# Kernel optimization log

Measured on AMD Instinct MI355X. Metric: run time of the kernel, lower is better.

## Reference

```python
import jax, jax.numpy as jnp
import numpy as np

S, DIM, H = 2048, 1024, 16
D = DIM // H  # head_dim = 64


def rope_rotate_half(x):
    x1, x2 = jnp.split(x, 2, axis=-1)
    return jnp.concatenate([-x2, x1], axis=-1)


def setup_inputs() -> dict:
    key = jax.random.key(0)
    ks = jax.random.split(key, 8)
    x = jax.random.normal(ks[0], (S, DIM), dtype=jnp.float32)
    # RoPE tables for full sequence (HW == S, prefix == 0)
    pos = jnp.arange(S, dtype=jnp.float32)[:, None]
    inv_freq = 1.0 / (10000.0 ** (jnp.arange(0, D, 2, dtype=jnp.float32) / D))
    ang = pos * inv_freq[None, :]                      # [S, D/2]
    ang = jnp.concatenate([ang, ang], axis=-1)         # [S, D]
    sin, cos = jnp.sin(ang), jnp.cos(ang)
    # equinox Linear: weight [out, in], y = W @ x + b
    W_qkv = jax.random.normal(ks[1], (3 * DIM, DIM), dtype=jnp.float32) * (DIM ** -0.5)
    b_qkv = jnp.zeros((3 * DIM,), dtype=jnp.float32)
    W_proj = jax.random.normal(ks[2], (DIM, DIM), dtype=jnp.float32) * (DIM ** -0.5)
    b_proj = jnp.zeros((DIM,), dtype=jnp.float32)
    return {"x": x, "sin": sin, "cos": cos, "W_qkv": W_qkv, "b_qkv": b_qkv,
            "W_proj": W_proj, "b_proj": b_proj}


def reference(x, sin, cos, W_qkv, b_qkv, W_proj, b_proj):
    # fused QKV projection: [S, 3*DIM]
    qkv = x @ W_qkv.T + b_qkv
    # 's (n h d) -> n h s d'
    qkv = qkv.reshape(S, 3, H, D).transpose(1, 2, 0, 3)
    q, k, v = qkv[0], qkv[1], qkv[2]                   # each [H, S, D]
    # qk_norm = False -> Identity. RoPE over all S tokens (prefix = 0).
    sin_b, cos_b = sin[None, :, :], cos[None, :, :]    # [1, S, D]
    q = q * cos_b + rope_rotate_half(q) * sin_b
    k = k * cos_b + rope_rotate_half(k) * sin_b
    attn = jnp.einsum('hqd,hkd->hqk', q, k) / jnp.sqrt(jnp.float32(D))
    attn = jax.nn.softmax(attn, axis=-1)               # [H, S, S]
    out = jnp.einsum('hqk,hkd->hqd', attn, v)          # [H, S, D]
    out = out.transpose(1, 0, 2).reshape(S, DIM)       # 'h s d -> s (h d)'
    return out @ W_proj.T + b_proj
```

## Files before the change

kernel.cpp:

```cpp
#include <hip/hip_runtime.h>

#define S_LEN 2048
#define DIM 1024
#define NH 16
#define HD 64
#define KSPLIT 4

typedef __attribute__((ext_vector_type(8))) __bf16 bf16x8;
typedef __attribute__((ext_vector_type(4))) _Float16 f16x4;
typedef __attribute__((ext_vector_type(4))) float f32x4;
typedef __attribute__((ext_vector_type(8))) unsigned short us8;
typedef __attribute__((ext_vector_type(4))) unsigned short us4;

__device__ __forceinline__ unsigned short f2bf(float f) {
    union { float f; unsigned u; } v; v.f = f;
    unsigned r = v.u + 0x7FFFu + ((v.u >> 16) & 1u);
    return (unsigned short)(r >> 16);
}
__device__ __forceinline__ float bf2f(unsigned short h) {
    union { unsigned u; float f; } v; v.u = ((unsigned)h) << 16;
    return v.f;
}
__device__ __forceinline__ f32x4 mfma16(bf16x8 a, bf16x8 b, f32x4 c) {
    return __builtin_amdgcn_mfma_f32_16x16x32_bf16(a, b, c, 0, 0, 0);
}
__device__ __forceinline__ f32x4 mfma16h(f16x4 a, f16x4 b, f32x4 c) {
    return __builtin_amdgcn_mfma_f32_16x16x16f16(a, b, c, 0, 0, 0);
}
__device__ __forceinline__ void gload_lds16(void* lds, const void* g) {
    __builtin_amdgcn_global_load_lds(
        (__attribute__((address_space(1))) void*)const_cast<void*>(g),
        (__attribute__((address_space(3))) void*)lds, 16, 0, 0);
}

__global__ __launch_bounds__(256) void convert2_kernel(
    const float* __restrict__ a, unsigned short* __restrict__ oa,
    const float* __restrict__ b, unsigned short* __restrict__ ob)
{
    const int bid = blockIdx.x;
    const float* in;
    unsigned short* out;
    int i;
    if (bid < 1024) { in = a; out = oa; i = (bid * 256 + threadIdx.x) * 8; }
    else            { in = b; out = ob; i = ((bid - 1024) * 256 + threadIdx.x) * 8; }
    const float4 p = *(const float4*)(in + i);
    const float4 q = *(const float4*)(in + i + 4);
    us8 o;
    o[0] = f2bf(p.x); o[1] = f2bf(p.y); o[2] = f2bf(p.z); o[3] = f2bf(p.w);
    o[4] = f2bf(q.x); o[5] = f2bf(q.y); o[6] = f2bf(q.z); o[7] = f2bf(q.w);
    *(us8*)(out + i) = o;
}

__global__ __launch_bounds__(256) void gemm_qkv_kernel(
    const unsigned short* __restrict__ A, const unsigned short* __restrict__ B,
    const float* __restrict__ bias, unsigned short* __restrict__ C,
    int M, int N, int K)
{
    __shared__ __align__(16) unsigned short As[128 * 32];
    __shared__ __align__(16) unsigned short Bs[64 * 32];

    const int tid  = threadIdx.x;
    const int w    = tid >> 6;
    const int lane = tid & 63;
    const int quad = lane >> 4;
    const int l15  = lane & 15;
    const int bm = blockIdx.y * 128, bn = blockIdx.x * 64;
    const int wm = w * 32;
    const int srow = lane >> 2;
    const int skc  = (lane & 3) * 8;

    f32x4 acc[2][4];
    const f32x4 zero4 = {0.f, 0.f, 0.f, 0.f};
    #pragma unroll
    for (int i = 0; i < 2; ++i)
        #pragma unroll
        for (int j = 0; j < 4; ++j) acc[i][j] = zero4;

    for (int k0 = 0; k0 < K; k0 += 32) {
        __syncthreads();
        #pragma unroll
        for (int t = 0; t < 2; ++t) {
            const int row = w * 32 + t * 16 + srow;
            gload_lds16(&As[(w * 32 + t * 16) * 32],
                        A + (size_t)(bm + row) * K + k0 + skc);
        }
        gload_lds16(&Bs[(w * 16) * 32],
                    B + (size_t)(bn + w * 16 + srow) * K + k0 + skc);
        __syncthreads();

        bf16x8 a[2], b[4];
        #pragma unroll
        for (int i = 0; i < 2; ++i)
            a[i] = *(const bf16x8*)&As[(wm + 16 * i + l15) * 32 + quad * 8];
        #pragma unroll
        for (int j = 0; j < 4; ++j)
            b[j] = *(const bf16x8*)&Bs[(16 * j + l15) * 32 + quad * 8];
        #pragma unroll
        for (int i = 0; i < 2; ++i)
            #pragma unroll
            for (int j = 0; j < 4; ++j)
                acc[i][j] = mfma16(a[i], b[j], acc[i][j]);
    }

    #pragma unroll
    for (int j = 0; j < 4; ++j) {
        const int col = bn + 16 * j + l15;
        const float bv = bias[col];
        #pragma unroll
        for (int i = 0; i < 2; ++i)
            #pragma unroll
            for (int r = 0; r < 4; ++r) {
                const int row = bm + wm + 16 * i + quad * 4 + r;
                C[(size_t)row * N + col] = f2bf(acc[i][j][r] + bv);
            }
    }
}

__global__ __launch_bounds__(256) void rope_vtrans_kernel(
    unsigned short* __restrict__ qkv, const float* __restrict__ sin_t,
    const float* __restrict__ cos_t, _Float16* __restrict__ Vt)
{
    const int bid = blockIdx.x;
    if (bid < 8192) {
        const int idx = bid * 256 + threadIdx.x;
        const int s  = idx >> 10;
        const int r  = idx & 1023;
        const int qk = r >> 9;
        const int h  = (r >> 5) & 15;
        const int d  = r & 31;
        const size_t base = (size_t)s * (3 * DIM) + qk * DIM + h * HD + d;
        const float a = bf2f(qkv[base]);
        const float b = bf2f(qkv[base + 32]);
        const float sv = sin_t[s * HD + d];
        const float cv = cos_t[s * HD + d];
        float ra = a * cv - b * sv;
        float rb = b * cv + a * sv;
        if (!qk) { ra *= 0.125f; rb *= 0.125f; }
        qkv[base]      = f2bf(ra);
        qkv[base + 32] = f2bf(rb);
    } else {
        const int vb = bid - 8192;
        const int h  = vb >> 7;
        const int sb = (vb & 127) * 16;
        const int d  = threadIdx.x & 63;
        const int sc = threadIdx.x >> 6;
        const int s0 = sb + sc * 4;
        f16x4 o;
        #pragma unroll
        for (int i = 0; i < 4; ++i)
            o[i] = (_Float16)bf2f(
                qkv[(size_t)(s0 + i) * (3 * DIM) + 2 * DIM + h * HD + d]);
        *(f16x4*)&Vt[(size_t)h * HD * S_LEN + (size_t)d * S_LEN + s0] = o;
    }
}

__global__ __launch_bounds__(256, 4) void attn_mfma_kernel(
    const unsigned short* __restrict__ qkv, const unsigned short* __restrict__ VtU,
    unsigned short* __restrict__ Opart, float* __restrict__ Lpart)
{
    __shared__ __align__(16) unsigned short Ks[64 * 64];
    __shared__ __align__(16) unsigned short Vts[64 * 64];

    const int h   = blockIdx.y;
    const int qb  = blockIdx.x * 128;
    const int ks  = blockIdx.z;
    const int kb0 = ks * (S_LEN / KSPLIT);
    const int tid  = threadIdx.x;
    const int w    = tid >> 6;
    const int lane = tid & 63;
    const int quad = lane >> 4;
    const int l15  = lane & 15;
    const int t7   = l15 & 7;
    const size_t hoff = (size_t)h * S_LEN * HD;

    bf16x8 aq[2][2];
    #pragma unroll
    for (int g = 0; g < 2; ++g)
        #pragma unroll
        for (int c = 0; c < 2; ++c)
            aq[g][c] = *(const bf16x8*)
                &qkv[(size_t)(qb + w * 32 + g * 16 + l15) * (3 * DIM) +
                     h * HD + 32 * c + quad * 8];

    const f32x4 zero4 = {0.f, 0.f, 0.f, 0.f};
    f32x4 o[2][4];
    #pragma unroll
    for (int g = 0; g < 2; ++g)
        #pragma unroll
        for (int dt = 0; dt < 4; ++dt) o[g][dt] = zero4;
    float lsum[2] = {0.f, 0.f};

    const int r0 = tid >> 3;
    const int c0 = tid & 7;

    us8 pk[2], pv[2];
    #pragma unroll
    for (int i = 0; i < 2; ++i) {
        const int row = r0 + 32 * i;
        pk[i] = *(const us8*)&qkv[(size_t)(kb0 + row) * (3 * DIM) +
                                  DIM + h * HD + c0 * 8];
        pv[i] = *(const us8*)&VtU[hoff + (size_t)row * S_LEN + kb0 + c0 * 8];
    }

    for (int kb = 0; kb < S_LEN / KSPLIT; kb += 64) {
        __syncthreads();
        #pragma unroll
        for (int i = 0; i < 2; ++i) {
            const int row = r0 + 32 * i;
            const int sw  = ((c0 ^ (row & 7)) << 3);
            *(us8*)&Ks[row * 64 + sw]  = pk[i];
            *(us8*)&Vts[row * 64 + sw] = pv[i];
        }
        __syncthreads();

        if (kb + 64 < S_LEN / KSPLIT) {
            #pragma unroll
            for (int i = 0; i < 2; ++i) {
                const int row = r0 + 32 * i;
                pk[i] = *(const us8*)&qkv[(size_t)(kb0 + kb + 64 + row) * (3 * DIM) +
                                          DIM + h * HD + c0 * 8];
                pv[i] = *(const us8*)&VtU[hoff + (size_t)row * S_LEN +
                                          kb0 + kb + 64 + c0 * 8];
            }
        }

        const _Float16* VtsH = (const _Float16*)Vts;
        #pragma unroll
        for (int g = 0; g < 2; ++g) {
            f32x4 s[4];
            #pragma unroll
            for (int kt = 0; kt < 4; ++kt) s[kt] = zero4;
            #pragma unroll
            for (int c = 0; c < 2; ++c)
                #pragma unroll
                for (int kt = 0; kt < 4; ++kt) {
                    const bf16x8 kf = *(const bf16x8*)
                        &Ks[(16 * kt + l15) * 64 + (((4 * c + quad) ^ t7) << 3)];
                    s[kt] = mfma16(kf, aq[g][c], s[kt]);
                }

            f16x4 pb[4];
            #pragma unroll
            for (int kt = 0; kt < 4; ++kt)
                #pragma unroll
                for (int r = 0; r < 4; ++r) {
                    const float p = __expf(s[kt][r]);
                    lsum[g] += p;
                    pb[kt][r] = (_Float16)p;
                }

            #pragma unroll
            for (int kt = 0; kt < 4; ++kt)
                #pragma unroll
                for (int dt = 0; dt < 4; ++dt) {
                    const f16x4 vf = *(const f16x4*)
                        &VtsH[(16 * dt + l15) * 64 +
                              (((2 * kt + (quad >> 1)) ^ t7) << 3) + (quad & 1) * 4];
                    o[g][dt] = mfma16h(pb[kt], vf, o[g][dt]);
                }
        }
    }

    #pragma unroll
    for (int g = 0; g < 2; ++g) {
        lsum[g] += __shfl_xor(lsum[g], 16);
        lsum[g] += __shfl_xor(lsum[g], 32);
        if (lane < 16)
            Lpart[((size_t)ks * NH + h) * S_LEN + qb + w * 32 + g * 16 + l15] = lsum[g];
    }

    #pragma unroll
    for (int g = 0; g < 2; ++g)
        #pragma unroll
        for (int dt = 0; dt < 4; ++dt)
            #pragma unroll
            for (int r = 0; r < 4; ++r) {
                const int row = qb + w * 32 + g * 16 + quad * 4 + r;
                Opart[(size_t)ks * S_LEN * DIM + (size_t)row * DIM +
                      h * HD + 16 * dt + l15] = f2bf(o[g][dt][r]);
            }
}

__global__ __launch_bounds__(256) void combine_kernel(
    const unsigned short* __restrict__ Opart, const float* __restrict__ Lpart,
    unsigned short* __restrict__ outb,
    const float* __restrict__ Wp, unsigned short* __restrict__ wp_bf)
{
    const int bid = blockIdx.x;
    if (bid < 2048) {
        const int idx = (bid * 256 + threadIdx.x) * 4;
        const int q = idx >> 10, col = idx & 1023, h = col >> 6;
        float l = 0.f;
        float v0 = 0.f, v1 = 0.f, v2 = 0.f, v3 = 0.f;
        #pragma unroll
        for (int ks = 0; ks < KSPLIT; ++ks) {
            l += Lpart[((size_t)ks * NH + h) * S_LEN + q];
            const us4 a = *(const us4*)(Opart + (size_t)ks * S_LEN * DIM + idx);
            v0 += bf2f(a[0]); v1 += bf2f(a[1]); v2 += bf2f(a[2]); v3 += bf2f(a[3]);
        }
        const float rl = 1.0f / l;
        us4 ob;
        ob[0] = f2bf(v0 * rl); ob[1] = f2bf(v1 * rl);
        ob[2] = f2bf(v2 * rl); ob[3] = f2bf(v3 * rl);
        *(us4*)(outb + idx) = ob;
    } else {
        const int i = ((bid - 2048) * 256 + threadIdx.x) * 8;
        const float4 p = *(const float4*)(Wp + i);
        const float4 q = *(const float4*)(Wp + i + 4);
        us8 o;
        o[0] = f2bf(p.x); o[1] = f2bf(p.y); o[2] = f2bf(p.z); o[3] = f2bf(p.w);
        o[4] = f2bf(q.x); o[5] = f2bf(q.y); o[6] = f2bf(q.z); o[7] = f2bf(q.w);
        *(us8*)(wp_bf + i) = o;
    }
}

__global__ __launch_bounds__(256) void gemm_proj_kernel(
    const unsigned short* __restrict__ A, const unsigned short* __restrict__ B,
    const float* __restrict__ bias, float* __restrict__ C,
    int M, int N, int K)
{
    __shared__ __align__(16) unsigned short As[64 * 32];
    __shared__ __align__(16) unsigned short Bs[64 * 32];

    const int tid  = threadIdx.x;
    const int w    = tid >> 6;
    const int lane = tid & 63;
    const int quad = lane >> 4;
    const int l15  = lane & 15;
    const int bm = blockIdx.y * 64, bn = blockIdx.x * 64;
    const int srow = lane >> 2;
    const int skc  = (lane & 3) * 8;

    f32x4 acc[4];
    const f32x4 zero4 = {0.f, 0.f, 0.f, 0.f};
    #pragma unroll
    for (int j = 0; j < 4; ++j) acc[j] = zero4;

    for (int k0 = 0; k0 < K; k0 += 32) {
        __syncthreads();
        {
            const int row = w * 16 + srow;
            gload_lds16(&As[(w * 16) * 32], A + (size_t)(bm + row) * K + k0 + skc);
            gload_lds16(&Bs[(w * 16) * 32], B + (size_t)(bn + row) * K + k0 + skc);
        }
        __syncthreads();

        bf16x8 a, b[4];
        a = *(const bf16x8*)&As[(w * 16 + l15) * 32 + quad * 8];
        #pragma unroll
        for (int j = 0; j < 4; ++j)
            b[j] = *(const bf16x8*)&Bs[(16 * j + l15) * 32 + quad * 8];
        #pragma unroll
        for (int j = 0; j < 4; ++j)
            acc[j] = mfma16(a, b[j], acc[j]);
    }

    #pragma unroll
    for (int j = 0; j < 4; ++j) {
        const int col = bn + 16 * j + l15;
        const float bv = bias[col];
        #pragma unroll
        for (int r = 0; r < 4; ++r) {
            const int row = bm + w * 16 + quad * 4 + r;
            C[(size_t)row * N + col] = acc[j][r] + bv;
        }
    }
}

extern "C" void kernel_launch(void* const* d_in, const int* in_sizes, int n_in,
                              void* d_out, int out_size, void* d_ws, size_t ws_size,
                              hipStream_t stream) {
    const float* x      = (const float*)d_in[0];
    const float* sin_t  = (const float*)d_in[1];
    const float* cos_t  = (const float*)d_in[2];
    const float* W_qkv  = (const float*)d_in[3];
    const float* b_qkv  = (const float*)d_in[4];
    const float* W_proj = (const float*)d_in[5];
    const float* b_proj = (const float*)d_in[6];
    float* out = (float*)d_out;

    char* ws = (char*)d_ws;
    unsigned short* qkv_bf = (unsigned short*)(ws);
    _Float16*       Vtbf   = (_Float16*)     (ws + 12582912);
    unsigned short* Opart  = (unsigned short*)(ws + 16777216);
    float*          Lpart  = (float*)        (ws + 33554432);
    unsigned short* a_bf   = (unsigned short*)(ws + 34078720);
    unsigned short* x_bf   = (unsigned short*)(ws + 38273024);
    unsigned short* wp_bf  = (unsigned short*)(ws + 38273024);
    unsigned short* wq_bf  = (unsigned short*)(ws + 42467328);

    const dim3 blk(256);

    convert2_kernel<<<dim3(2560), blk, 0, stream>>>(x, x_bf, W_qkv, wq_bf);

    gemm_qkv_kernel<<<dim3(48, 16), blk, 0, stream>>>(
        x_bf, wq_bf, b_qkv, qkv_bf, S_LEN, 3 * DIM, DIM);

    rope_vtrans_kernel<<<dim3(10240), blk, 0, stream>>>(
        qkv_bf, sin_t, cos_t, Vtbf);

    attn_mfma_kernel<<<dim3(16, NH, KSPLIT), blk, 0, stream>>>(
        qkv_bf, (const unsigned short*)Vtbf, Opart, Lpart);

    combine_kernel<<<dim3(2560), blk, 0, stream>>>(
        Opart, Lpart, a_bf, W_proj, wp_bf);

    gemm_proj_kernel<<<dim3(16, 32), blk, 0, stream>>>(
        a_bf, wp_bf, b_proj, out, S_LEN, DIM, DIM);
}
```

Measured before the change: 165.2 us.

## Fuse RoPE and V transpose into QKV GEMM epilogue, swizzle LDS tiles

Folds the RoPE rotation, Q scaling and the V transpose to fp16 into the QKV GEMM epilogue, which removes the separate rope_vtrans kernel and its round trip through global memory. The QKV GEMM moves to 128x128 tiles with 64x64 per-warp subtiles and XOR-swizzled LDS layouts. The projection GEMM now uses a K step of 64 with a swizzled LDS layout. The costs are more registers per thread in the QKV GEMM, fewer blocks launched (384), and scattered two-byte stores in the epilogue.

Result: faster. 150.9 us (-8.6%).

```diff
diff --git a/kernel.cpp b/kernel.cpp
--- a/kernel.cpp
+++ b/kernel.cpp
@@ -31,6 +31,13 @@
     __builtin_amdgcn_global_load_lds(
         (__attribute__((address_space(1))) void*)const_cast<void*>(g),
         (__attribute__((address_space(3))) void*)lds, 16, 0, 0);
+}
+__device__ __forceinline__ int sw32(int row, int c) {
+    const int p = row >> 1;
+    return (p * 8 + ((((row & 1) << 2) | c) ^ (p & 7))) * 8;
+}
+__device__ __forceinline__ int sw64(int row, int c) {
+    return (row * 8 + (c ^ (row & 7))) * 8;
 }
 
 __global__ __launch_bounds__(256) void convert2_kernel(
@@ -51,28 +58,33 @@
     *(us8*)(out + i) = o;
 }
 
-__global__ __launch_bounds__(256) void gemm_qkv_kernel(
+__global__ __launch_bounds__(256) void gemm_qkv_fused_kernel(
     const unsigned short* __restrict__ A, const unsigned short* __restrict__ B,
-    const float* __restrict__ bias, unsigned short* __restrict__ C,
-    int M, int N, int K)
+    const float* __restrict__ bias, const float* __restrict__ sin_t,
+    const float* __restrict__ cos_t, unsigned short* __restrict__ qkv,
+    _Float16* __restrict__ Vt)
 {
     __shared__ __align__(16) unsigned short As[128 * 32];
-    __shared__ __align__(16) unsigned short Bs[64 * 32];
+    __shared__ __align__(16) unsigned short Bs[128 * 32];
 
     const int tid  = threadIdx.x;
     const int w    = tid >> 6;
     const int lane = tid & 63;
     const int quad = lane >> 4;
     const int l15  = lane & 15;
-    const int bm = blockIdx.y * 128, bn = blockIdx.x * 64;
-    const int wm = w * 32;
-    const int srow = lane >> 2;
-    const int skc  = (lane & 3) * 8;
-
-    f32x4 acc[2][4];
+    const int bm = blockIdx.y * 128, bn = blockIdx.x * 128;
+    const int wm = (w >> 1) * 64,    wn = (w & 1) * 64;
+    const int K = DIM;
+
+    const int pl   = lane >> 3;
+    const int tt   = (lane & 7) ^ pl;
+    const int srow = (pl << 1) | (tt >> 2);
+    const int skc  = (tt & 3) << 3;
+
+    f32x4 acc[4][4];
     const f32x4 zero4 = {0.f, 0.f, 0.f, 0.f};
     #pragma unroll
-    for (int i = 0; i < 2; ++i)
+    for (int i = 0; i < 4; ++i)
         #pragma unroll
         for (int j = 0; j < 4; ++j) acc[i][j] = zero4;
 
@@ -80,77 +92,68 @@
         __syncthreads();
         #pragma unroll
         for (int t = 0; t < 2; ++t) {
-            const int row = w * 32 + t * 16 + srow;
-            gload_lds16(&As[(w * 32 + t * 16) * 32],
-                        A + (size_t)(bm + row) * K + k0 + skc);
-        }
-        gload_lds16(&Bs[(w * 16) * 32],
-                    B + (size_t)(bn + w * 16 + srow) * K + k0 + skc);
-        __syncthreads();
-
-        bf16x8 a[2], b[4];
-        #pragma unroll
-        for (int i = 0; i < 2; ++i)
-            a[i] = *(const bf16x8*)&As[(wm + 16 * i + l15) * 32 + quad * 8];
-        #pragma unroll
-        for (int j = 0; j < 4; ++j)
-            b[j] = *(const bf16x8*)&Bs[(16 * j + l15) * 32 + quad * 8];
-        #pragma unroll
-        for (int i = 0; i < 2; ++i)
+            const int R0 = w * 32 + t * 16;
+            gload_lds16(&As[R0 * 32], A + (size_t)(bm + R0 + srow) * K + k0 + skc);
+            gload_lds16(&Bs[R0 * 32], B + (size_t)(bn + R0 + srow) * K + k0 + skc);
+        }
+        __syncthreads();
+
+        bf16x8 a[4], b[4];
+        #pragma unroll
+        for (int i = 0; i < 4; ++i) {
+            a[i] = *(const bf16x8*)&As[sw32(wm + 16 * i + l15, quad)];
+            b[i] = *(const bf16x8*)&Bs[sw32(wn + 16 * i + l15, quad)];
+        }
+        #pragma unroll
+        for (int i = 0; i < 4; ++i)
             #pragma unroll
             for (int j = 0; j < 4; ++j)
                 acc[i][j] = mfma16(a[i], b[j], acc[i][j]);
     }
 
-    #pragma unroll
-    for (int j = 0; j < 4; ++j) {
-        const int col = bn + 16 * j + l15;
-        const float bv = bias[col];
-        #pragma unroll
-        for (int i = 0; i < 2; ++i)
+    const int sec = blockIdx.x >> 3;
+    float bv[4];
+    #pragma unroll
+    for (int j = 0; j < 4; ++j) bv[j] = bias[bn + wn + 16 * j + l15];
+
+    if (sec < 2) {
+        const float scale = (sec == 0) ? 0.125f : 1.0f;
+        const int colb = bn + wn + l15;
+        #pragma unroll
+        for (int i = 0; i < 4; ++i)
             #pragma unroll
             for (int r = 0; r < 4; ++r) {
                 const int row = bm + wm + 16 * i + quad * 4 + r;
-                C[(size_t)row * N + col] = f2bf(acc[i][j][r] + bv);
+                const float cv0 = cos_t[row * 64 + l15];
+                const float sv0 = sin_t[row * 64 + l15];
+                const float cv1 = cos_t[row * 64 + 16 + l15];
+                const float sv1 = sin_t[row * 64 + 16 + l15];
+                const float v0 = acc[i][0][r] + bv[0];
+                const float v1 = acc[i][1][r] + bv[1];
+                const float v2 = acc[i][2][r] + bv[2];
+                const float v3 = acc[i][3][r] + bv[3];
+                unsigned short* dst = qkv + (size_t)row * (3 * DIM) + colb;
+                dst[0]  = f2bf((v0 * cv0 - v2 * sv0) * scale);
+                dst[16] = f2bf((v1 * cv1 - v3 * sv1) * scale);
+                dst[32] = f2bf((v2 * cv0 + v0 * sv0) * scale);
+                dst[48] = f2bf((v3 * cv1 + v1 * sv1) * scale);
             }
-    }
-}
-
-__global__ __launch_bounds__(256) void rope_vtrans_kernel(
-    unsigned short* __restrict__ qkv, const float* __restrict__ sin_t,
-    const float* __restrict__ cos_t, _Float16* __restrict__ Vt)
-{
-    const int bid = blockIdx.x;
-    if (bid < 8192) {
-        const int idx = bid * 256 + threadIdx.x;
-        const int s  = idx >> 10;
-        const int r  = idx & 1023;
-        const int qk = r >> 9;
-        const int h  = (r >> 5) & 15;
-        const int d  = r & 31;
-        const size_t base = (size_t)s * (3 * DIM) + qk * DIM + h * HD + d;
-        const float a = bf2f(qkv[base]);
-        const float b = bf2f(qkv[base + 32]);
-        const float sv = sin_t[s * HD + d];
-        const float cv = cos_t[s * HD + d];
-        float ra = a * cv - b * sv;
-        float rb = b * cv + a * sv;
-        if (!qk) { ra *= 0.125f; rb *= 0.125f; }
-        qkv[base]      = f2bf(ra);
-        qkv[base + 32] = f2bf(rb);
     } else {
-        const int vb = bid - 8192;
-        const int h  = vb >> 7;
-        const int sb = (vb & 127) * 16;
-        const int d  = threadIdx.x & 63;
-        const int sc = threadIdx.x >> 6;
-        const int s0 = sb + sc * 4;
-        f16x4 o;
-        #pragma unroll
-        for (int i = 0; i < 4; ++i)
-            o[i] = (_Float16)bf2f(
-                qkv[(size_t)(s0 + i) * (3 * DIM) + 2 * DIM + h * HD + d]);
-        *(f16x4*)&Vt[(size_t)h * HD * S_LEN + (size_t)d * S_LEN + s0] = o;
+        const int vcolb = (blockIdx.x - 16) * 128 + wn;
+        #pragma unroll
+        for (int j = 0; j < 4; ++j) {
+            const int vcol = vcolb + 16 * j + l15;
+            const int h = vcol >> 6, d = vcol & 63;
+            #pragma unroll
+            for (int i = 0; i < 4; ++i) {
+                const int s0 = bm + wm + 16 * i + quad * 4;
+                f16x4 o;
+                #pragma unroll
+                for (int r = 0; r < 4; ++r)
+                    o[r] = (_Float16)(acc[i][j][r] + bv[j]);
+                *(f16x4*)&Vt[(size_t)h * HD * S_LEN + (size_t)d * S_LEN + s0] = o;
+            }
+        }
     }
 }
 
@@ -319,8 +322,8 @@
     const float* __restrict__ bias, float* __restrict__ C,
     int M, int N, int K)
 {
-    __shared__ __align__(16) unsigned short As[64 * 32];
-    __shared__ __align__(16) unsigned short Bs[64 * 32];
+    __shared__ __align__(16) unsigned short As[64 * 64];
+    __shared__ __align__(16) unsigned short Bs[64 * 64];
 
     const int tid  = threadIdx.x;
     const int w    = tid >> 6;
@@ -328,31 +331,34 @@
     const int quad = lane >> 4;
     const int l15  = lane & 15;
     const int bm = blockIdx.y * 64, bn = blockIdx.x * 64;
-    const int srow = lane >> 2;
-    const int skc  = (lane & 3) * 8;
 
     f32x4 acc[4];
     const f32x4 zero4 = {0.f, 0.f, 0.f, 0.f};
     #pragma unroll
     for (int j = 0; j < 4; ++j) acc[j] = zero4;
 
-    for (int k0 = 0; k0 < K; k0 += 32) {
-        __syncthreads();
-        {
-            const int row = w * 16 + srow;
-            gload_lds16(&As[(w * 16) * 32], A + (size_t)(bm + row) * K + k0 + skc);
-            gload_lds16(&Bs[(w * 16) * 32], B + (size_t)(bn + row) * K + k0 + skc);
-        }
-        __syncthreads();
-
-        bf16x8 a, b[4];
-        a = *(const bf16x8*)&As[(w * 16 + l15) * 32 + quad * 8];
-        #pragma unroll
-        for (int j = 0; j < 4; ++j)
-            b[j] = *(const bf16x8*)&Bs[(16 * j + l15) * 32 + quad * 8];
-        #pragma unroll
-        for (int j = 0; j < 4; ++j)
-            acc[j] = mfma16(a, b[j], acc[j]);
+    for (int k0 = 0; k0 < K; k0 += 64) {
+        __syncthreads();
+        #pragma unroll
+        for (int i2 = 0; i2 < 2; ++i2) {
+            const int CI  = i2 * 256 + tid;
+            const int row = CI >> 3;
+            const int c   = (CI & 7) ^ (row & 7);
+            const int base = (i2 * 256 + w * 64) * 8;
+            gload_lds16(&As[base], A + (size_t)(bm + row) * K + k0 + c * 8);
+            gload_lds16(&Bs[base], B + (size_t)(bn + row) * K + k0 + c * 8);
+        }
+        __syncthreads();
+
+        #pragma unroll
+        for (int c32 = 0; c32 < 2; ++c32) {
+            const bf16x8 a = *(const bf16x8*)&As[sw64(w * 16 + l15, c32 * 4 + quad)];
+            #pragma unroll
+            for (int j = 0; j < 4; ++j) {
+                const bf16x8 b = *(const bf16x8*)&Bs[sw64(16 * j + l15, c32 * 4 + quad)];
+                acc[j] = mfma16(a, b, acc[j]);
+            }
+        }
     }
 
     #pragma unroll
@@ -393,11 +399,8 @@
 
     convert2_kernel<<<dim3(2560), blk, 0, stream>>>(x, x_bf, W_qkv, wq_bf);
 
-    gemm_qkv_kernel<<<dim3(48, 16), blk, 0, stream>>>(
-        x_bf, wq_bf, b_qkv, qkv_bf, S_LEN, 3 * DIM, DIM);
-
-    rope_vtrans_kernel<<<dim3(10240), blk, 0, stream>>>(
-        qkv_bf, sin_t, cos_t, Vtbf);
+    gemm_qkv_fused_kernel<<<dim3(24, 16), blk, 0, stream>>>(
+        x_bf, wq_bf, b_qkv, sin_t, cos_t, qkv_bf, Vtbf);
 
     attn_mfma_kernel<<<dim3(16, NH, KSPLIT), blk, 0, stream>>>(
         qkv_bf, (const unsigned short*)Vtbf, Opart, Lpart);
```
